# Optimization experiments

Hardware: AMD Instinct MI355X
Metric: run time of the kernel (lower is better)

The kernel has to match this reference:

```python
import jax, jax.numpy as jnp
import numpy as np

B, T, C, H = 4, 1024, 768, 12
HD = C // H  # 64
EPS = 1e-5

def setup_inputs() -> dict:
    key = jax.random.key(0)
    ks = jax.random.split(key, 6)
    s = 0.02
    return {
        "x": jax.random.normal(ks[0], (B, T, C), jnp.float32),
        "ln1_w": jnp.ones((C,), jnp.float32),
        "w_attn": jax.random.normal(ks[1], (C, 3 * C), jnp.float32) * s,
        "w_pos": jax.random.normal(ks[2], (C, C), jnp.float32) * s,
        "w_cproj": jax.random.normal(ks[3], (C, C), jnp.float32) * s,
        "ln2_w": jnp.ones((C,), jnp.float32),
        "w_fc": jax.random.normal(ks[4], (C, 4 * C), jnp.float32) * s,
        "w_mproj": jax.random.normal(ks[5], (4 * C, C), jnp.float32) * s,
    }

def _layernorm(x, w):
    m = jnp.mean(x, axis=-1, keepdims=True)
    v = jnp.mean(jnp.square(x - m), axis=-1, keepdims=True)
    return (x - m) * jax.lax.rsqrt(v + EPS) * w

def _rpe_table(dtype):
    # sinusoidal table over relative distances [-(T-1), T-1] -> [2T-1, HD]
    inv_freq = 1.0 / (10000.0 ** (jnp.arange(0, HD, 2, dtype=jnp.float32) / HD))
    dist = jnp.arange(-(T - 1), T, dtype=jnp.float32)
    freqs = dist[:, None] * inv_freq[None, :]
    return jnp.concatenate([jnp.sin(freqs), jnp.cos(freqs)], axis=-1).astype(dtype)

def reference(x, ln1_w, w_attn, w_pos, w_cproj, ln2_w, w_fc, w_mproj):
    # ---- attention branch ----
    h = _layernorm(x, ln1_w)
    qkv = h @ w_attn                                 # [B,T,3C]
    q, k, v = jnp.split(qkv, 3, axis=-1)
    q = q.reshape(B, T, H, HD).transpose(0, 2, 1, 3)  # [B,H,T,HD]
    k = k.reshape(B, T, H, HD).transpose(0, 2, 1, 3)
    v = v.reshape(B, T, H, HD).transpose(0, 2, 1, 3)
    # note: the original also computes p = c_pos(x) but never uses it (dead code)

    # relative position embeddings gathered to [T,T,HD]
    idx = jnp.arange(T)
    rel = jnp.clip(idx[:, None] - idx[None, :], -(T - 1), T - 1) + (T - 1)
    rpe = _rpe_table(q.dtype)[rel]                    # [T,T,HD]

    scale = 1.0 / np.sqrt(HD)
    att = (jnp.einsum('bhid,bhjd->bhij', q, k)
           + jnp.einsum('bhid,ijd->bhij', q, rpe)) * scale
    causal = idx[:, None] >= idx[None, :]             # [T,T] lower-tri
    att = jnp.where(causal, att, -jnp.inf)
    att = jax.nn.softmax(att, axis=-1)
    y = jnp.einsum('bhij,bhjd->bhid', att, v)         # [B,H,T,HD]
    y = y.transpose(0, 2, 1, 3).reshape(B, T, C) @ w_cproj
    x = x + y

    # ---- MLP branch ----
    h2 = _layernorm(x, ln2_w)
    m = jax.nn.gelu(h2 @ w_fc, approximate=False) @ w_mproj
    return x + m
```

## Files before the change

kernel.cpp:

```cpp
#include <hip/hip_runtime.h>
#include <math.h>

typedef __attribute__((ext_vector_type(8))) short bf16x8;
typedef __attribute__((ext_vector_type(4))) float f32x4;
typedef __attribute__((ext_vector_type(16))) float f32x16;
typedef __attribute__((ext_vector_type(4))) unsigned u32x4;

__device__ inline short f2bf(float f) {
  unsigned u = __builtin_bit_cast(unsigned, f);
  u = u + 0x7fffu + ((u >> 16) & 1u);
  return (short)(u >> 16);
}
__device__ inline float bf2f(short s) {
  return __builtin_bit_cast(float, ((unsigned)(unsigned short)s) << 16);
}
__device__ inline unsigned cvt_pk_bf16(float lo, float hi) {
  unsigned r;
  asm("v_cvt_pk_bf16_f32 %0, %1, %2" : "=v"(r) : "v"(lo), "v"(hi));
  return r;
}

__device__ inline void gload16(const short* g, short* l) {
  __builtin_amdgcn_global_load_lds(
      (const __attribute__((address_space(1))) unsigned*)g,
      (__attribute__((address_space(3))) unsigned*)l, 16, 0, 0);
}

__global__ __launch_bounds__(256) void wtrans_all(
    const float* __restrict__ wa, const float* __restrict__ wc,
    const float* __restrict__ wf, const float* __restrict__ wm,
    short* __restrict__ oa, short* __restrict__ oc,
    short* __restrict__ of, short* __restrict__ om) {
  __shared__ float tile[32][33];
  int blk = blockIdx.x;
  const float* in; short* out; int K, N, bx;
  if (blk < 1728)      { in = wa; out = oa; K = 768;  N = 2304; bx = 72; }
  else if (blk < 2304) { blk -= 1728; in = wc; out = oc; K = 768;  N = 768;  bx = 24; }
  else if (blk < 4608) { blk -= 2304; in = wf; out = of; K = 768;  N = 3072; bx = 96; }
  else                 { blk -= 4608; in = wm; out = om; K = 3072; N = 768;  bx = 24; }
  const int n0 = (blk % bx) * 32, k0 = (blk / bx) * 32;
  const int tx = threadIdx.x & 31, ty = threadIdx.x >> 5;
  #pragma unroll
  for (int r = ty; r < 32; r += 8)
    tile[r][tx] = in[(size_t)(k0 + r) * N + n0 + tx];
  __syncthreads();
  #pragma unroll
  for (int r = ty; r < 32; r += 8)
    out[(size_t)(n0 + r) * K + k0 + tx] = f2bf(tile[tx][r]);
}

__global__ __launch_bounds__(256) void qprime_kernel(
    const short* __restrict__ qkv, short* __restrict__ qpr,
    short* __restrict__ ktab) {
  const int idx = blockIdx.x * 256 + threadIdx.x;
  const int cc = idx & 31;
  const int row = idx >> 5;
  const int i = row & 1023, bh = row >> 10;
  const int b = bh / 12, h = bh % 12;
  const float invf = exp2f(-(float)cc * (13.287712379549449f / 32.0f));
  const float ang = (float)i * invf;
  float si, co;
  __sincosf(ang, &si, &co);
  if (bh == 0) {
    ktab[i * 64 + cc]      = f2bf(co);
    ktab[i * 64 + 32 + cc] = f2bf(si);
  }
  const short* q = qkv + (size_t)(b * 1024 + i) * 2304 + h * 64;
  const float qs = bf2f(q[cc]), qc = bf2f(q[32 + cc]);
  qpr[(size_t)row * 64 + cc]      = f2bf(qs * si + qc * co);
  qpr[(size_t)row * 64 + 32 + cc] = f2bf(qc * si - qs * co);
}

__global__ __launch_bounds__(256) void ln_kernel(
    const float* __restrict__ x, const float* __restrict__ w,
    short* __restrict__ out) {
  const int row = blockIdx.x, tid = threadIdx.x;
  const float* xr = x + (size_t)row * 768;
  float v0 = xr[tid], v1 = xr[tid + 256], v2 = xr[tid + 512];
  float s = v0 + v1 + v2;
  #pragma unroll
  for (int o = 1; o < 64; o <<= 1) s += __shfl_xor(s, o);
  __shared__ float red[8];
  const int wv = tid >> 6;
  if ((tid & 63) == 0) red[wv] = s;
  __syncthreads();
  const float mean = (red[0] + red[1] + red[2] + red[3]) * (1.0f / 768.0f);
  v0 -= mean; v1 -= mean; v2 -= mean;
  float q = v0 * v0 + v1 * v1 + v2 * v2;
  #pragma unroll
  for (int o = 1; o < 64; o <<= 1) q += __shfl_xor(q, o);
  if ((tid & 63) == 0) red[4 + wv] = q;
  __syncthreads();
  const float var = (red[4] + red[5] + red[6] + red[7]) * (1.0f / 768.0f);
  const float inv = 1.0f / sqrtf(var + 1e-5f);
  out[(size_t)row * 768 + tid]       = f2bf(v0 * inv * w[tid]);
  out[(size_t)row * 768 + tid + 256] = f2bf(v1 * inv * w[tid + 256]);
  out[(size_t)row * 768 + tid + 512] = f2bf(v2 * inv * w[tid + 512]);
}

__global__ __launch_bounds__(256) void vtrans_kernel(
    const short* __restrict__ qkv, short* __restrict__ vT) {
  __shared__ short tile[64][65];
  const int blk = blockIdx.x;
  const int bh = blk >> 4, t0 = (blk & 15) * 64;
  const int b = bh / 12, h = bh % 12;
  const int tx = threadIdx.x & 63, ty = threadIdx.x >> 6;
  const short* src = qkv + (size_t)(b * 1024 + t0) * 2304 + 1536 + h * 64;
  #pragma unroll
  for (int r = ty; r < 64; r += 4)
    tile[r][tx] = src[(size_t)r * 2304 + tx];
  __syncthreads();
  short* dst = vT + (size_t)bh * 64 * 1024 + t0;
  #pragma unroll
  for (int r = ty; r < 64; r += 4)
    dst[(size_t)r * 1024 + tx] = tile[tx][r];
}

template <int EPI, int BM, int BN>
__global__ __launch_bounds__(256) void gemm_bt(
    const short* __restrict__ A, const short* __restrict__ Bt,
    const float* __restrict__ res, float* __restrict__ outF,
    short* __restrict__ outB, int M, int N, int K, int lda, int ldb) {
  __shared__ __align__(16) short As[2][BM * 32];
  __shared__ __align__(16) short Bs[2][BN * 32];
  constexpr int WM = BM / 2, WN = BN / 2;
  constexpr int MI = WM / 16, NJ = WN / 16;
  const int tid = threadIdx.x;
  const int w = tid >> 6, lane = tid & 63;
  const int gx = gridDim.x, gy = gridDim.y;
  const int nwg = gx * gy * gridDim.z;
  const int lin = blockIdx.x + gx * (blockIdx.y + gy * blockIdx.z);
  const int wg = (lin & 7) * (nwg >> 3) + (lin >> 3);
  const int bxi = wg % gx;
  const int tmp = wg / gx;
  const int byi = tmp % gy;
  const int bzi = tmp / gy;
  const int m0 = byi * BM, n0 = bxi * BN;
  const int wm = (w >> 1) * WM, wn = (w & 1) * WN;
  const int lr = lane >> 2;
  const int lc = (lane & 3) * 8;
  if constexpr (EPI == 3) {
    A += (size_t)bzi * K;
    Bt += (size_t)bzi * K;
    outF += (size_t)bzi * M * N;
  }
  f32x4 acc[MI][NJ];
  #pragma unroll
  for (int i = 0; i < MI; i++)
    #pragma unroll
    for (int j = 0; j < NJ; j++)
      #pragma unroll
      for (int r = 0; r < 4; r++) acc[i][j][r] = 0.0f;

  const int nt = K / 32;
  #pragma unroll
  for (int p = 0; p < BM / 64; ++p)
    gload16(A + (size_t)(m0 + p * 64 + w * 16 + lr) * lda + lc,
            &As[0][p * 2048 + w * 512]);
  #pragma unroll
  for (int p = 0; p < BN / 64; ++p)
    gload16(Bt + (size_t)(n0 + p * 64 + w * 16 + lr) * ldb + lc,
            &Bs[0][p * 2048 + w * 512]);
  __syncthreads();

  for (int t = 0; t < nt; ++t) {
    const int cur = t & 1;
    if (t + 1 < nt) {
      const int kt = (t + 1) * 32;
      #pragma unroll
      for (int p = 0; p < BM / 64; ++p)
        gload16(A + (size_t)(m0 + p * 64 + w * 16 + lr) * lda + kt + lc,
                &As[cur ^ 1][p * 2048 + w * 512]);
      #pragma unroll
      for (int p = 0; p < BN / 64; ++p)
        gload16(Bt + (size_t)(n0 + p * 64 + w * 16 + lr) * ldb + kt + lc,
                &Bs[cur ^ 1][p * 2048 + w * 512]);
    }
    bf16x8 af[MI], bfr[NJ];
    #pragma unroll
    for (int i = 0; i < MI; i++)
      af[i] = *(const bf16x8*)&As[cur][(wm + i * 16 + (lane & 15)) * 32 + (lane >> 4) * 8];
    #pragma unroll
    for (int j = 0; j < NJ; j++)
      bfr[j] = *(const bf16x8*)&Bs[cur][(wn + j * 16 + (lane & 15)) * 32 + (lane >> 4) * 8];
    #pragma unroll
    for (int i = 0; i < MI; i++)
      #pragma unroll
      for (int j = 0; j < NJ; j++)
        acc[i][j] = __builtin_amdgcn_mfma_f32_16x16x32_bf16(af[i], bfr[j],
                                                            acc[i][j], 0, 0, 0);
    __syncthreads();
  }
  const int r0 = (lane >> 4) * 4, cl = lane & 15;
  #pragma unroll
  for (int i = 0; i < MI; i++) {
    #pragma unroll
    for (int j = 0; j < NJ; j++) {
      const int gm = m0 + wm + i * 16 + r0;
      const int gn = n0 + wn + j * 16 + cl;
      #pragma unroll
      for (int r = 0; r < 4; r++) {
        const size_t idx = (size_t)(gm + r) * N + gn;
        const float v = acc[i][j][r];
        if constexpr (EPI == 0) {
          outB[idx] = f2bf(v);
        } else if constexpr (EPI == 1) {
          outF[idx] = res[idx] + v;
        } else if constexpr (EPI == 2) {
          outB[idx] = f2bf(0.5f * v * (1.0f + erff(v * 0.70710678118f)));
        } else {
          outF[idx] = v;
        }
      }
    }
  }
}

__global__ __launch_bounds__(256) void reduce_splitk(
    const float* __restrict__ Cp, const float* __restrict__ res,
    float* __restrict__ out) {
  const size_t i4 = ((size_t)blockIdx.x * 256 + threadIdx.x) * 4;
  float4 a = *(const float4*)(res + i4);
  #pragma unroll
  for (int z = 0; z < 2; ++z) {
    float4 p = *(const float4*)(Cp + (size_t)z * 3145728 + i4);
    a.x += p.x; a.y += p.y; a.z += p.z; a.w += p.w;
  }
  *(float4*)(out + i4) = a;
}

__global__ __launch_bounds__(512) void attn_part8(
    const short* __restrict__ qkv, const short* __restrict__ vT,
    const short* __restrict__ qpr, const short* __restrict__ ktab,
    float* __restrict__ mpart, float* __restrict__ lpart,
    short* __restrict__ Ypart) {
  __shared__ __align__(16) short Ka[2][32 * 136];
  __shared__ __align__(16) short Va[2][64 * 40];
  const int bx = blockIdx.x;
  const int bh = bx / 20;
  const int r = bx % 20;
  int c, sub;
  if (r < 4)        { c = 0; sub = r; }
  else if (r < 8)   { c = 1; sub = r - 4; }
  else if (r < 11)  { c = 2; sub = r - 8; }
  else if (r < 14)  { c = 3; sub = r - 11; }
  else if (r < 16)  { c = 4; sub = r - 14; }
  else if (r < 18)  { c = 5; sub = r - 16; }
  else if (r == 18) { c = 6; sub = 0; }
  else              { c = 7; sub = 0; }
  const int tid = threadIdx.x;
  const int w = tid >> 6;
  const int lane = tid & 63;
  const int li = lane & 31, hi = lane >> 5;
  const int it = 4 * c + sub * 8 + w;
  const bool valid = (it <= 31);
  const int b = bh / 12, h = bh % 12;
  const int I0 = (valid ? it : 31) * 32;
  const int jt0 = 4 * c;
  const int jtmax = valid ? ((it < jt0 + 3) ? it : jt0 + 3) : (jt0 - 1);
  constexpr float SCALE2 = 0.125f * 1.44269504089f;

  const short* kbase = qkv + (size_t)(b * 1024) * 2304 + 768 + h * 64;
  const short* vbase = vT + (size_t)bh * 64 * 1024;

  const int krow = tid >> 4, kch = tid & 15;
  const short* ksrc = (kch < 8) ? (kbase + kch * 8) : (ktab + (kch - 8) * 8);
  const size_t kstr = (kch < 8) ? 2304 : 64;
  const int vrow = tid >> 2, vch = tid & 3;

  int4 kreg, vreg;
  {
    const int J0 = jt0 * 32;
    kreg = *(const int4*)(ksrc + (size_t)(J0 + krow) * kstr);
    if (tid < 256)
      vreg = *(const int4*)(vbase + (size_t)vrow * 1024 + J0 + vch * 8);
  }

  const short* qrow = qkv + (size_t)(b * 1024 + I0 + li) * 2304 + h * 64;
  const short* qprow = qpr + ((size_t)bh * 1024 + I0 + li) * 64;
  bf16x8 qf[8];
  #pragma unroll
  for (int s = 0; s < 4; s++) {
    qf[s]     = *(const bf16x8*)(qrow + s * 16 + hi * 8);
    qf[4 + s] = *(const bf16x8*)(qprow + s * 16 + hi * 8);
  }

  *(int4*)&Ka[0][krow * 136 + kch * 8] = kreg;
  if (tid < 256) *(int4*)&Va[0][vrow * 40 + vch * 8] = vreg;
  __syncthreads();

  float m_run = -1e30f, l_run = 0.0f;
  f32x16 ya0, ya1;
  #pragma unroll
  for (int q = 0; q < 16; q++) { ya0[q] = 0.0f; ya1[q] = 0.0f; }

  for (int t = 0; t < 4; ++t) {
    const int cur = t & 1;
    if (t < 3) {
      const int J0n = (jt0 + t + 1) * 32;
      kreg = *(const int4*)(ksrc + (size_t)(J0n + krow) * kstr);
      if (tid < 256)
        vreg = *(const int4*)(vbase + (size_t)vrow * 1024 + J0n + vch * 8);
    }
    const int jt = jt0 + t;
    if (jt <= jtmax) {
      bf16x8 kf[8];
      #pragma unroll
      for (int s = 0; s < 8; s++)
        kf[s] = *(const bf16x8*)&Ka[cur][li * 136 + s * 16 + hi * 8];
      bf16x8 vc[4];
      #pragma unroll
      for (int s = 0; s < 2; s++) {
        vc[s * 2]     = *(const bf16x8*)&Va[cur][li * 40 + s * 16 + hi * 8];
        vc[s * 2 + 1] = *(const bf16x8*)&Va[cur][(32 + li) * 40 + s * 16 + hi * 8];
      }
      f32x16 sa0, sa1;
      #pragma unroll
      for (int q = 0; q < 16; q++) { sa0[q] = 0.0f; sa1[q] = 0.0f; }
      __builtin_amdgcn_s_setprio(1);
      #pragma unroll
      for (int s = 0; s < 4; s++) {
        sa0 = __builtin_amdgcn_mfma_f32_32x32x16_bf16(kf[2 * s],     qf[2 * s],     sa0, 0, 0, 0);
        sa1 = __builtin_amdgcn_mfma_f32_32x32x16_bf16(kf[2 * s + 1], qf[2 * s + 1], sa1, 0, 0, 0);
      }
      __builtin_amdgcn_s_setprio(0);
      float sv[16];
      float mx = -1e30f;
      if (jt == it) {
        #pragma unroll
        for (int q = 0; q < 16; q++) {
          const int j = (q & 3) + 8 * (q >> 2) + 4 * hi;
          float v = (sa0[q] + sa1[q]) * SCALE2;
          v = (j <= li) ? v : -1e30f;
          sv[q] = v;
          mx = fmaxf(mx, v);
        }
      } else {
        #pragma unroll
        for (int q = 0; q < 16; q++) {
          const float v = (sa0[q] + sa1[q]) * SCALE2;
          sv[q] = v;
          mx = fmaxf(mx, v);
        }
      }
      mx = fmaxf(mx, __shfl_xor(mx, 32));
      float mref = m_run;
      float alpha = 1.0f;
      const bool resc = !__all(mx <= m_run + 11.5f);
      if (resc) {
        mref = fmaxf(m_run, mx);
        alpha = exp2f(m_run - mref);
        m_run = mref;
      }
      float psum = 0.0f;
      unsigned pw[8];
      #pragma unroll
      for (int q = 0; q < 8; q++) {
        const float p0 = exp2f(sv[2 * q] - mref);
        const float p1 = exp2f(sv[2 * q + 1] - mref);
        psum += p0 + p1;
        pw[q] = cvt_pk_bf16(p0, p1);
      }
      psum += __shfl_xor(psum, 32);
      l_run = l_run * alpha + psum;
      if (resc) {
        #pragma unroll
        for (int q = 0; q < 16; q++) {
          const int row = (q & 3) + 8 * (q >> 2) + 4 * hi;
          const float a = __shfl(alpha, row);
          ya0[q] *= a;
          ya1[q] *= a;
        }
      }
      #pragma unroll
      for (int s = 0; s < 2; s++) {
        unsigned a0 = pw[4 * s],     b0 = pw[4 * s + 2];
        unsigned a1 = pw[4 * s + 1], b1 = pw[4 * s + 3];
        asm volatile("v_permlane32_swap_b32 %0, %1" : "+v"(a0), "+v"(b0));
        asm volatile("v_permlane32_swap_b32 %0, %1" : "+v"(a1), "+v"(b1));
        u32x4 t4;
        t4[0] = a0; t4[1] = a1; t4[2] = b0; t4[3] = b1;
        const bf16x8 pf = __builtin_bit_cast(bf16x8, t4);
        __builtin_amdgcn_s_setprio(1);
        ya0 = __builtin_amdgcn_mfma_f32_32x32x16_bf16(pf, vc[s * 2],     ya0, 0, 0, 0);
        ya1 = __builtin_amdgcn_mfma_f32_32x32x16_bf16(pf, vc[s * 2 + 1], ya1, 0, 0, 0);
        __builtin_amdgcn_s_setprio(0);
      }
    }
    if (t < 3) {
      *(int4*)&Ka[cur ^ 1][krow * 136 + kch * 8] = kreg;
      if (tid < 256) *(int4*)&Va[cur ^ 1][vrow * 40 + vch * 8] = vreg;
    }
    __syncthreads();
  }
  if (!valid) return;
  const int task = bh * 144 + it + 30 * c - 2 * c * c;
  if (hi == 0) {
    mpart[(size_t)task * 32 + li] = m_run;
    lpart[(size_t)task * 32 + li] = l_run;
  }
  short* yb = Ypart + (size_t)task * 2048;
  #pragma unroll
  for (int q = 0; q < 16; q++) {
    const int row = (q & 3) + 8 * (q >> 2) + 4 * hi;
    yb[row * 64 + li]      = f2bf(ya0[q]);
    yb[row * 64 + 32 + li] = f2bf(ya1[q]);
  }
}

__global__ __launch_bounds__(256) void attn_combine(
    const float* __restrict__ mpart, const float* __restrict__ lpart,
    const short* __restrict__ Ypart, short* __restrict__ yout) {
  const int blk = blockIdx.x;
  const int it = blk & 31, bh = blk >> 5;
  const int b = bh / 12, h = bh % 12;
  const int g = it >> 2;
  const int nc = g + 1;
  const int row = threadIdx.x >> 3;
  const int c0 = (threadIdx.x & 7) * 8;
  float mv[8], lv[8], wgt[8];
  float m = -1e30f;
  #pragma unroll
  for (int cI = 0; cI < 8; ++cI) {
    const int idx = bh * 144 + it + 30 * cI - 2 * cI * cI;
    mv[cI] = (cI < nc) ? mpart[(size_t)idx * 32 + row] : -1e30f;
    lv[cI] = (cI < nc) ? lpart[(size_t)idx * 32 + row] : 0.0f;
    m = fmaxf(m, mv[cI]);
  }
  float L = 0.0f;
  #pragma unroll
  for (int cI = 0; cI < 8; ++cI) {
    wgt[cI] = exp2f(mv[cI] - m);
    L += lv[cI] * wgt[cI];
  }
  const float inv = 1.0f / L;
  float y[8];
  #pragma unroll
  for (int r = 0; r < 8; r++) y[r] = 0.0f;
  #pragma unroll
  for (int cI = 0; cI < 8; ++cI) {
    if (cI < nc) {
      const int idx = bh * 144 + it + 30 * cI - 2 * cI * cI;
      bf16x8 v = *(const bf16x8*)(Ypart + ((size_t)idx * 32 + row) * 64 + c0);
      #pragma unroll
      for (int r = 0; r < 8; r++) y[r] += bf2f(v[r]) * wgt[cI];
    }
  }
  short* dst = yout + (size_t)(b * 1024 + it * 32 + row) * 768 + h * 64 + c0;
  #pragma unroll
  for (int r = 0; r < 8; r++) dst[r] = f2bf(y[r] * inv);
}

extern "C" void kernel_launch(void* const* d_in, const int* in_sizes, int n_in,
                              void* d_out, int out_size, void* d_ws, size_t ws_size,
                              hipStream_t stream) {
  const float* x       = (const float*)d_in[0];
  const float* ln1_w   = (const float*)d_in[1];
  const float* w_attn  = (const float*)d_in[2];
  const float* w_cproj = (const float*)d_in[4];
  const float* ln2_w   = (const float*)d_in[5];
  const float* w_fc    = (const float*)d_in[6];
  const float* w_mproj = (const float*)d_in[7];
  float* out = (float*)d_out;
  char* ws = (char*)d_ws;

  short* wT_attn  = (short*)(ws + 0);
  short* wT_cproj = (short*)(ws + 3538944);
  short* wT_fc    = (short*)(ws + 4718592);
  short* wT_mproj = (short*)(ws + 9437184);
  short* ktab     = (short*)(ws + 14155776);
  short* h_bf     = (short*)(ws + 14417920);
  short* qpr      = (short*)(ws + 14417920);
  short* qkv_bf   = (short*)(ws + 20709376);
  short* vT       = (short*)(ws + 39583744);
  short* y_att    = (short*)(ws + 45875200);
  short* h2_bf    = (short*)(ws + 52166656);
  short* hfc_bf   = (short*)(ws + 58458112);
  float* mpart = (float*)(ws + 52166656);
  float* lpart = (float*)(ws + 53051392);
  short* Ypart = (short*)(ws + 53936128);
  float* Cpart = (float*)(ws + 20709376);

  wtrans_all<<<6912, 256, 0, stream>>>(w_attn, w_cproj, w_fc, w_mproj,
                                       wT_attn, wT_cproj, wT_fc, wT_mproj);

  ln_kernel<<<4096, 256, 0, stream>>>(x, ln1_w, h_bf);
  gemm_bt<0, 128, 128><<<dim3(18, 32), 256, 0, stream>>>(
      h_bf, wT_attn, nullptr, nullptr, qkv_bf, 4096, 2304, 768, 768, 768);
  qprime_kernel<<<6144, 256, 0, stream>>>(qkv_bf, qpr, ktab);
  vtrans_kernel<<<768, 256, 0, stream>>>(qkv_bf, vT);
  attn_part8<<<960, 512, 0, stream>>>(qkv_bf, vT, qpr, ktab, mpart, lpart, Ypart);
  attn_combine<<<1536, 256, 0, stream>>>(mpart, lpart, Ypart, y_att);
  gemm_bt<1, 64, 64><<<dim3(12, 64), 256, 0, stream>>>(
      y_att, wT_cproj, x, out, nullptr, 4096, 768, 768, 768, 768);
  ln_kernel<<<4096, 256, 0, stream>>>(out, ln2_w, h2_bf);
  gemm_bt<2, 128, 128><<<dim3(24, 32), 256, 0, stream>>>(
      h2_bf, wT_fc, nullptr, nullptr, hfc_bf, 4096, 3072, 768, 768, 768);
  gemm_bt<3, 128, 64><<<dim3(12, 32, 2), 256, 0, stream>>>(
      hfc_bf, wT_mproj, nullptr, Cpart, nullptr, 4096, 768, 1536, 3072, 3072);
  reduce_splitk<<<3072, 256, 0, stream>>>(Cpart, out, out);
}
```

Measured before the change: 200.7 us.

## Add 256x256 eight-wave pipelined GEMM for QKV, FC and split-K MLP projection

Adds a new 512-thread GEMM kernel with 256x256 output tiles, 64-wide K steps, XOR-swizzled double-buffered LDS loaded through global_load_lds, and an eight-phase schedule that interleaves LDS fragment reads, next-tile staging and MFMA with explicit waitcnt and priority hints. The QKV, FC and MLP-down GEMMs now use it, and the MLP-down split-K goes from 2 to 3 partitions to keep enough workgroups with the larger tiles. The aim is more operand reuse per LDS byte and better overlap of loads with math. The cost is fewer workgroups, for example 144 for QKV, which may underfill the CU count, plus heavy register use for the 8x4 accumulator array and an extra partial buffer to reduce.

```diff
diff --git a/kernel.cpp b/kernel.cpp
--- a/kernel.cpp
+++ b/kernel.cpp
@@ -20,10 +20,10 @@
   return r;
 }
 
-__device__ inline void gload16(const short* g, short* l) {
+__device__ inline void gload16(const short* g, const short* l) {
   __builtin_amdgcn_global_load_lds(
       (const __attribute__((address_space(1))) unsigned*)g,
-      (__attribute__((address_space(3))) unsigned*)l, 16, 0, 0);
+      (__attribute__((address_space(3))) unsigned*)(short*)l, 16, 0, 0);
 }
 
 __global__ __launch_bounds__(256) void wtrans_all(
@@ -114,6 +114,149 @@
   #pragma unroll
   for (int r = ty; r < 64; r += 4)
     dst[(size_t)r * 1024 + tx] = tile[tx][r];
+}
+
+template <int EPI>
+__global__ __launch_bounds__(512) void gemm8(
+    const short* __restrict__ A, const short* __restrict__ Bt,
+    float* __restrict__ outF, short* __restrict__ outB,
+    int M, int N, int K, int lda, int ldb) {
+  __shared__ __align__(16) short lds[65536];
+  const int tid = threadIdx.x;
+  const int w = tid >> 6, lane = tid & 63;
+  const int gx = gridDim.x, gy = gridDim.y;
+  const int nwg = gx * gy * gridDim.z;
+  const int lin = blockIdx.x + gx * (blockIdx.y + gy * blockIdx.z);
+  const int wg = (lin & 7) * (nwg >> 3) + (lin >> 3);
+  const int bxi = wg % gx;
+  const int tmp = wg / gx;
+  const int byi = tmp % gy, bzi = tmp / gy;
+  const int m0 = byi * 256, n0 = bxi * 256;
+  if constexpr (EPI == 3) {
+    A += (size_t)bzi * K;
+    Bt += (size_t)bzi * K;
+    outF += (size_t)bzi * (size_t)M * N;
+  }
+  const int wm = (w >> 2) * 128, wn = (w & 3) * 64;
+
+  f32x4 acc[8][4];
+  #pragma unroll
+  for (int i = 0; i < 8; i++)
+    #pragma unroll
+    for (int j = 0; j < 4; j++)
+      #pragma unroll
+      for (int r = 0; r < 4; r++) acc[i][j][r] = 0.0f;
+
+  const int nt = K >> 6;
+  const int niter = nt >> 1;
+  const int spmax = nt * 4;
+  const int wbase = (tid & ~63);
+
+  auto stage_seq = [&](int ht) {
+    const int tile = ht >> 2;
+    const int part = ht & 3;
+    const int kofs = tile * 64;
+    const int dbo = (tile & 1) * 16384;
+    const short* P;
+    int ld, rbase, roff;
+    if (part == 0)      { P = Bt; ld = ldb; rbase = n0;       roff = 32768 + dbo; }
+    else if (part == 1) { P = Bt; ld = ldb; rbase = n0 + 128; roff = 32768 + dbo + 8192; }
+    else if (part == 2) { P = A;  ld = lda; rbase = m0;       roff = dbo; }
+    else                { P = A;  ld = lda; rbase = m0 + 128; roff = dbo + 8192; }
+    #pragma unroll
+    for (int p = 0; p < 2; ++p) {
+      const int c = p * 512 + tid;
+      const int row = c >> 3;
+      const int scc = ((c & 7) ^ (row & 7)) * 8;
+      gload16(P + (size_t)(rbase + row) * ld + kofs + scc,
+              lds + roff + (p * 512 + wbase) * 8);
+    }
+  };
+
+  bf16x8 af[4][2];
+  bf16x8 bq[2][2][2];
+
+  int sp = 0;
+  for (; sp < 6; ++sp) stage_seq(sp);
+  asm volatile("s_waitcnt vmcnt(4)" ::: "memory");
+  __builtin_amdgcn_sched_barrier(0);
+  __builtin_amdgcn_s_barrier();
+
+#define GPHASE(DB, QM, QN, LA, LB, VMKIND)                                     \
+  {                                                                            \
+    if (LA) {                                                                  \
+      _Pragma("unroll") for (int i = 0; i < 4; i++)                            \
+        _Pragma("unroll") for (int ks = 0; ks < 2; ks++) {                     \
+          const int rr = wm + QM * 64 + i * 16 + (lane & 15);                  \
+          const int c4 = ks * 4 + (lane >> 4);                                 \
+          af[i][ks] = *(const bf16x8*)&lds[DB * 16384 + rr * 64 +              \
+                                           ((c4 ^ (rr & 7)) * 8)];             \
+        }                                                                      \
+    }                                                                          \
+    if (LB) {                                                                  \
+      _Pragma("unroll") for (int j = 0; j < 2; j++)                            \
+        _Pragma("unroll") for (int ks = 0; ks < 2; ks++) {                     \
+          const int rr = wn + QN * 32 + j * 16 + (lane & 15);                  \
+          const int c4 = ks * 4 + (lane >> 4);                                 \
+          bq[QN][j][ks] = *(const bf16x8*)&lds[32768 + DB * 16384 + rr * 64 +  \
+                                               ((c4 ^ (rr & 7)) * 8)];         \
+        }                                                                      \
+    }                                                                          \
+    if (sp < spmax) { stage_seq(sp); ++sp; }                                   \
+    __builtin_amdgcn_s_barrier();                                              \
+    asm volatile("s_waitcnt lgkmcnt(0)" ::: "memory");                         \
+    __builtin_amdgcn_sched_barrier(0);                                         \
+    __builtin_amdgcn_s_setprio(1);                                             \
+    _Pragma("unroll") for (int i = 0; i < 4; i++)                              \
+      _Pragma("unroll") for (int j = 0; j < 2; j++)                            \
+        _Pragma("unroll") for (int ks = 0; ks < 2; ks++)                       \
+          acc[QM * 4 + i][QN * 2 + j] = __builtin_amdgcn_mfma_f32_16x16x32_bf16( \
+              af[i][ks], bq[QN][j][ks], acc[QM * 4 + i][QN * 2 + j], 0, 0, 0); \
+    __builtin_amdgcn_s_setprio(0);                                             \
+    if (VMKIND == 1) {                                                         \
+      if (it == niter - 1) asm volatile("s_waitcnt vmcnt(0)" ::: "memory");    \
+      else                 asm volatile("s_waitcnt vmcnt(4)" ::: "memory");    \
+      __builtin_amdgcn_sched_barrier(0);                                       \
+    } else if (VMKIND == 2) {                                                  \
+      if (it < niter - 1)  asm volatile("s_waitcnt vmcnt(4)" ::: "memory");    \
+      __builtin_amdgcn_sched_barrier(0);                                       \
+    }                                                                          \
+    __builtin_amdgcn_s_barrier();                                              \
+  }
+
+  for (int it = 0; it < niter; ++it) {
+    GPHASE(0, 0, 0, 1, 1, 0)
+    GPHASE(0, 0, 1, 0, 1, 0)
+    GPHASE(0, 1, 0, 1, 0, 0)
+    GPHASE(0, 1, 1, 0, 0, 1)
+    GPHASE(1, 0, 0, 1, 1, 0)
+    GPHASE(1, 0, 1, 0, 1, 0)
+    GPHASE(1, 1, 0, 1, 0, 0)
+    GPHASE(1, 1, 1, 0, 0, 2)
+  }
+#undef GPHASE
+
+  const int r0 = (lane >> 4) * 4, cl = lane & 15;
+  #pragma unroll
+  for (int I = 0; I < 8; I++) {
+    #pragma unroll
+    for (int J = 0; J < 4; J++) {
+      const int gm = m0 + wm + I * 16 + r0;
+      const int gn = n0 + wn + J * 16 + cl;
+      #pragma unroll
+      for (int r = 0; r < 4; r++) {
+        const size_t idx = (size_t)(gm + r) * N + gn;
+        const float v = acc[I][J][r];
+        if constexpr (EPI == 0) {
+          outB[idx] = f2bf(v);
+        } else if constexpr (EPI == 2) {
+          outB[idx] = f2bf(0.5f * v * (1.0f + erff(v * 0.70710678118f)));
+        } else {
+          outF[idx] = v;
+        }
+      }
+    }
+  }
 }
 
 template <int EPI, int BM, int BN>
@@ -134,16 +277,10 @@
   const int bxi = wg % gx;
   const int tmp = wg / gx;
   const int byi = tmp % gy;
-  const int bzi = tmp / gy;
   const int m0 = byi * BM, n0 = bxi * BN;
   const int wm = (w >> 1) * WM, wn = (w & 1) * WN;
   const int lr = lane >> 2;
   const int lc = (lane & 3) * 8;
-  if constexpr (EPI == 3) {
-    A += (size_t)bzi * K;
-    Bt += (size_t)bzi * K;
-    outF += (size_t)bzi * M * N;
-  }
   f32x4 acc[MI][NJ];
   #pragma unroll
   for (int i = 0; i < MI; i++)
@@ -202,14 +339,10 @@
       for (int r = 0; r < 4; r++) {
         const size_t idx = (size_t)(gm + r) * N + gn;
         const float v = acc[i][j][r];
-        if constexpr (EPI == 0) {
+        if constexpr (EPI == 1) {
+          outF[idx] = res[idx] + v;
+        } else {
           outB[idx] = f2bf(v);
-        } else if constexpr (EPI == 1) {
-          outF[idx] = res[idx] + v;
-        } else if constexpr (EPI == 2) {
-          outB[idx] = f2bf(0.5f * v * (1.0f + erff(v * 0.70710678118f)));
-        } else {
-          outF[idx] = v;
         }
       }
     }
@@ -222,7 +355,7 @@
   const size_t i4 = ((size_t)blockIdx.x * 256 + threadIdx.x) * 4;
   float4 a = *(const float4*)(res + i4);
   #pragma unroll
-  for (int z = 0; z < 2; ++z) {
+  for (int z = 0; z < 3; ++z) {
     float4 p = *(const float4*)(Cp + (size_t)z * 3145728 + i4);
     a.x += p.x; a.y += p.y; a.z += p.z; a.w += p.w;
   }
@@ -485,8 +618,8 @@
                                        wT_attn, wT_cproj, wT_fc, wT_mproj);
 
   ln_kernel<<<4096, 256, 0, stream>>>(x, ln1_w, h_bf);
-  gemm_bt<0, 128, 128><<<dim3(18, 32), 256, 0, stream>>>(
-      h_bf, wT_attn, nullptr, nullptr, qkv_bf, 4096, 2304, 768, 768, 768);
+  gemm8<0><<<dim3(9, 16), 512, 0, stream>>>(
+      h_bf, wT_attn, nullptr, qkv_bf, 4096, 2304, 768, 768, 768);
   qprime_kernel<<<6144, 256, 0, stream>>>(qkv_bf, qpr, ktab);
   vtrans_kernel<<<768, 256, 0, stream>>>(qkv_bf, vT);
   attn_part8<<<960, 512, 0, stream>>>(qkv_bf, vT, qpr, ktab, mpart, lpart, Ypart);
@@ -494,9 +627,9 @@
   gemm_bt<1, 64, 64><<<dim3(12, 64), 256, 0, stream>>>(
       y_att, wT_cproj, x, out, nullptr, 4096, 768, 768, 768, 768);
   ln_kernel<<<4096, 256, 0, stream>>>(out, ln2_w, h2_bf);
-  gemm_bt<2, 128, 128><<<dim3(24, 32), 256, 0, stream>>>(
-      h2_bf, wT_fc, nullptr, nullptr, hfc_bf, 4096, 3072, 768, 768, 768);
-  gemm_bt<3, 128, 64><<<dim3(12, 32, 2), 256, 0, stream>>>(
-      hfc_bf, wT_mproj, nullptr, Cpart, nullptr, 4096, 768, 1536, 3072, 3072);
+  gemm8<2><<<dim3(12, 16), 512, 0, stream>>>(
+      h2_bf, wT_fc, nullptr, hfc_bf, 4096, 3072, 768, 768, 768);
+  gemm8<3><<<dim3(3, 16, 3), 512, 0, stream>>>(
+      hfc_bf, wT_mproj, Cpart, nullptr, 4096, 768, 1024, 3072, 3072);
   reduce_splitk<<<3072, 256, 0, stream>>>(Cpart, out, out);
 }
```

Result: slower. 216.8 us (+8.0%).

## Triple-buffer GEMM LDS with one barrier per k-step; fuse qprime and V transpose

Applied to the files above, without the earlier changes.

The GEMM now keeps three LDS stages instead of two, prefetching two k-tiles ahead. Each iteration waits with a partial vmcnt and issues a single barrier, where the old loop synchronised twice per step. Separately, the qprime and V-transpose kernels are merged into one launch that branches on block index, saving a kernel launch. The costs are more shared memory per block, which may lower occupancy, and the correctness of the hand-placed waitcnt/barrier ordering, since the next stage is issued right after the LDS fragment reads.

```diff
diff --git a/kernel.cpp b/kernel.cpp
--- a/kernel.cpp
+++ b/kernel.cpp
@@ -20,10 +20,10 @@
   return r;
 }
 
-__device__ inline void gload16(const short* g, short* l) {
+__device__ inline void gload16(const short* g, const short* l) {
   __builtin_amdgcn_global_load_lds(
       (const __attribute__((address_space(1))) unsigned*)g,
-      (__attribute__((address_space(3))) unsigned*)l, 16, 0, 0);
+      (__attribute__((address_space(3))) unsigned*)(short*)l, 16, 0, 0);
 }
 
 __global__ __launch_bounds__(256) void wtrans_all(
@@ -49,26 +49,43 @@
     out[(size_t)(n0 + r) * K + k0 + tx] = f2bf(tile[tx][r]);
 }
 
-__global__ __launch_bounds__(256) void qprime_kernel(
+__global__ __launch_bounds__(256) void qv_kernel(
     const short* __restrict__ qkv, short* __restrict__ qpr,
-    short* __restrict__ ktab) {
-  const int idx = blockIdx.x * 256 + threadIdx.x;
-  const int cc = idx & 31;
-  const int row = idx >> 5;
-  const int i = row & 1023, bh = row >> 10;
-  const int b = bh / 12, h = bh % 12;
-  const float invf = exp2f(-(float)cc * (13.287712379549449f / 32.0f));
-  const float ang = (float)i * invf;
-  float si, co;
-  __sincosf(ang, &si, &co);
-  if (bh == 0) {
-    ktab[i * 64 + cc]      = f2bf(co);
-    ktab[i * 64 + 32 + cc] = f2bf(si);
-  }
-  const short* q = qkv + (size_t)(b * 1024 + i) * 2304 + h * 64;
-  const float qs = bf2f(q[cc]), qc = bf2f(q[32 + cc]);
-  qpr[(size_t)row * 64 + cc]      = f2bf(qs * si + qc * co);
-  qpr[(size_t)row * 64 + 32 + cc] = f2bf(qc * si - qs * co);
+    short* __restrict__ ktab, short* __restrict__ vT) {
+  __shared__ short tile[64][65];
+  if (blockIdx.x < 6144) {
+    const int idx = blockIdx.x * 256 + threadIdx.x;
+    const int cc = idx & 31;
+    const int row = idx >> 5;
+    const int i = row & 1023, bh = row >> 10;
+    const int b = bh / 12, h = bh % 12;
+    const float invf = exp2f(-(float)cc * (13.287712379549449f / 32.0f));
+    const float ang = (float)i * invf;
+    float si, co;
+    __sincosf(ang, &si, &co);
+    if (bh == 0) {
+      ktab[i * 64 + cc]      = f2bf(co);
+      ktab[i * 64 + 32 + cc] = f2bf(si);
+    }
+    const short* q = qkv + (size_t)(b * 1024 + i) * 2304 + h * 64;
+    const float qs = bf2f(q[cc]), qc = bf2f(q[32 + cc]);
+    qpr[(size_t)row * 64 + cc]      = f2bf(qs * si + qc * co);
+    qpr[(size_t)row * 64 + 32 + cc] = f2bf(qc * si - qs * co);
+  } else {
+    const int blk = blockIdx.x - 6144;
+    const int bh = blk >> 4, t0 = (blk & 15) * 64;
+    const int b = bh / 12, h = bh % 12;
+    const int tx = threadIdx.x & 63, ty = threadIdx.x >> 6;
+    const short* src = qkv + (size_t)(b * 1024 + t0) * 2304 + 1536 + h * 64;
+    #pragma unroll
+    for (int r = ty; r < 64; r += 4)
+      tile[r][tx] = src[(size_t)r * 2304 + tx];
+    __syncthreads();
+    short* dst = vT + (size_t)bh * 64 * 1024 + t0;
+    #pragma unroll
+    for (int r = ty; r < 64; r += 4)
+      dst[(size_t)r * 1024 + tx] = tile[tx][r];
+  }
 }
 
 __global__ __launch_bounds__(256) void ln_kernel(
@@ -98,33 +115,16 @@
   out[(size_t)row * 768 + tid + 512] = f2bf(v2 * inv * w[tid + 512]);
 }
 
-__global__ __launch_bounds__(256) void vtrans_kernel(
-    const short* __restrict__ qkv, short* __restrict__ vT) {
-  __shared__ short tile[64][65];
-  const int blk = blockIdx.x;
-  const int bh = blk >> 4, t0 = (blk & 15) * 64;
-  const int b = bh / 12, h = bh % 12;
-  const int tx = threadIdx.x & 63, ty = threadIdx.x >> 6;
-  const short* src = qkv + (size_t)(b * 1024 + t0) * 2304 + 1536 + h * 64;
-  #pragma unroll
-  for (int r = ty; r < 64; r += 4)
-    tile[r][tx] = src[(size_t)r * 2304 + tx];
-  __syncthreads();
-  short* dst = vT + (size_t)bh * 64 * 1024 + t0;
-  #pragma unroll
-  for (int r = ty; r < 64; r += 4)
-    dst[(size_t)r * 1024 + tx] = tile[tx][r];
-}
-
 template <int EPI, int BM, int BN>
-__global__ __launch_bounds__(256) void gemm_bt(
+__global__ __launch_bounds__(256) void gemm3b(
     const short* __restrict__ A, const short* __restrict__ Bt,
     const float* __restrict__ res, float* __restrict__ outF,
     short* __restrict__ outB, int M, int N, int K, int lda, int ldb) {
-  __shared__ __align__(16) short As[2][BM * 32];
-  __shared__ __align__(16) short Bs[2][BN * 32];
+  __shared__ __align__(16) short As[3][BM * 32];
+  __shared__ __align__(16) short Bs[3][BN * 32];
   constexpr int WM = BM / 2, WN = BN / 2;
   constexpr int MI = WM / 16, NJ = WN / 16;
+  constexpr int G = (BM + BN) / 64;
   const int tid = threadIdx.x;
   const int w = tid >> 6, lane = tid & 63;
   const int gx = gridDim.x, gy = gridDim.y;
@@ -133,8 +133,7 @@
   const int wg = (lin & 7) * (nwg >> 3) + (lin >> 3);
   const int bxi = wg % gx;
   const int tmp = wg / gx;
-  const int byi = tmp % gy;
-  const int bzi = tmp / gy;
+  const int byi = tmp % gy, bzi = tmp / gy;
   const int m0 = byi * BM, n0 = bxi * BN;
   const int wm = (w >> 1) * WM, wn = (w & 1) * WN;
   const int lr = lane >> 2;
@@ -142,7 +141,7 @@
   if constexpr (EPI == 3) {
     A += (size_t)bzi * K;
     Bt += (size_t)bzi * K;
-    outF += (size_t)bzi * M * N;
+    outF += (size_t)bzi * (size_t)M * N;
   }
   f32x4 acc[MI][NJ];
   #pragma unroll
@@ -153,44 +152,49 @@
       for (int r = 0; r < 4; r++) acc[i][j][r] = 0.0f;
 
   const int nt = K / 32;
-  #pragma unroll
-  for (int p = 0; p < BM / 64; ++p)
-    gload16(A + (size_t)(m0 + p * 64 + w * 16 + lr) * lda + lc,
-            &As[0][p * 2048 + w * 512]);
-  #pragma unroll
-  for (int p = 0; p < BN / 64; ++p)
-    gload16(Bt + (size_t)(n0 + p * 64 + w * 16 + lr) * ldb + lc,
-            &Bs[0][p * 2048 + w * 512]);
-  __syncthreads();
+
+  auto stage = [&](int t) {
+    const int kt = t * 32;
+    short* Ab = As[t % 3];
+    short* Bb = Bs[t % 3];
+    #pragma unroll
+    for (int p = 0; p < BM / 64; ++p)
+      gload16(A + (size_t)(m0 + p * 64 + w * 16 + lr) * lda + kt + lc,
+              Ab + p * 2048 + w * 512);
+    #pragma unroll
+    for (int p = 0; p < BN / 64; ++p)
+      gload16(Bt + (size_t)(n0 + p * 64 + w * 16 + lr) * ldb + kt + lc,
+              Bb + p * 2048 + w * 512);
+  };
+
+  stage(0);
+  if (nt > 1) stage(1);
 
   for (int t = 0; t < nt; ++t) {
-    const int cur = t & 1;
-    if (t + 1 < nt) {
-      const int kt = (t + 1) * 32;
-      #pragma unroll
-      for (int p = 0; p < BM / 64; ++p)
-        gload16(A + (size_t)(m0 + p * 64 + w * 16 + lr) * lda + kt + lc,
-                &As[cur ^ 1][p * 2048 + w * 512]);
-      #pragma unroll
-      for (int p = 0; p < BN / 64; ++p)
-        gload16(Bt + (size_t)(n0 + p * 64 + w * 16 + lr) * ldb + kt + lc,
-                &Bs[cur ^ 1][p * 2048 + w * 512]);
-    }
+    if (t < nt - 1)
+      asm volatile("s_waitcnt vmcnt(%0)" :: "n"(G) : "memory");
+    else
+      asm volatile("s_waitcnt vmcnt(0)" ::: "memory");
+    __builtin_amdgcn_s_barrier();
+    __builtin_amdgcn_sched_barrier(0);
+    const short* Ab = As[t % 3];
+    const short* Bb = Bs[t % 3];
     bf16x8 af[MI], bfr[NJ];
     #pragma unroll
     for (int i = 0; i < MI; i++)
-      af[i] = *(const bf16x8*)&As[cur][(wm + i * 16 + (lane & 15)) * 32 + (lane >> 4) * 8];
+      af[i] = *(const bf16x8*)&Ab[(wm + i * 16 + (lane & 15)) * 32 + (lane >> 4) * 8];
     #pragma unroll
     for (int j = 0; j < NJ; j++)
-      bfr[j] = *(const bf16x8*)&Bs[cur][(wn + j * 16 + (lane & 15)) * 32 + (lane >> 4) * 8];
+      bfr[j] = *(const bf16x8*)&Bb[(wn + j * 16 + (lane & 15)) * 32 + (lane >> 4) * 8];
+    if (t + 2 < nt) stage(t + 2);
     #pragma unroll
     for (int i = 0; i < MI; i++)
       #pragma unroll
       for (int j = 0; j < NJ; j++)
         acc[i][j] = __builtin_amdgcn_mfma_f32_16x16x32_bf16(af[i], bfr[j],
                                                             acc[i][j], 0, 0, 0);
-    __syncthreads();
-  }
+  }
+
   const int r0 = (lane >> 4) * 4, cl = lane & 15;
   #pragma unroll
   for (int i = 0; i < MI; i++) {
@@ -485,18 +489,17 @@
                                        wT_attn, wT_cproj, wT_fc, wT_mproj);
 
   ln_kernel<<<4096, 256, 0, stream>>>(x, ln1_w, h_bf);
-  gemm_bt<0, 128, 128><<<dim3(18, 32), 256, 0, stream>>>(
+  gemm3b<0, 128, 128><<<dim3(18, 32), 256, 0, stream>>>(
       h_bf, wT_attn, nullptr, nullptr, qkv_bf, 4096, 2304, 768, 768, 768);
-  qprime_kernel<<<6144, 256, 0, stream>>>(qkv_bf, qpr, ktab);
-  vtrans_kernel<<<768, 256, 0, stream>>>(qkv_bf, vT);
+  qv_kernel<<<6912, 256, 0, stream>>>(qkv_bf, qpr, ktab, vT);
   attn_part8<<<960, 512, 0, stream>>>(qkv_bf, vT, qpr, ktab, mpart, lpart, Ypart);
   attn_combine<<<1536, 256, 0, stream>>>(mpart, lpart, Ypart, y_att);
-  gemm_bt<1, 64, 64><<<dim3(12, 64), 256, 0, stream>>>(
+  gemm3b<1, 64, 64><<<dim3(12, 64), 256, 0, stream>>>(
       y_att, wT_cproj, x, out, nullptr, 4096, 768, 768, 768, 768);
   ln_kernel<<<4096, 256, 0, stream>>>(out, ln2_w, h2_bf);
-  gemm_bt<2, 128, 128><<<dim3(24, 32), 256, 0, stream>>>(
+  gemm3b<2, 128, 128><<<dim3(24, 32), 256, 0, stream>>>(
       h2_bf, wT_fc, nullptr, nullptr, hfc_bf, 4096, 3072, 768, 768, 768);
-  gemm_bt<3, 128, 64><<<dim3(12, 32, 2), 256, 0, stream>>>(
+  gemm3b<3, 128, 64><<<dim3(12, 32, 2), 256, 0, stream>>>(
       hfc_bf, wT_mproj, nullptr, Cpart, nullptr, 4096, 768, 1536, 3072, 3072);
   reduce_splitk<<<3072, 256, 0, stream>>>(Cpart, out, out);
 }
```

Result: faster. 194.4 us (-3.1%).
